# Performance work log

Measured on AMD Instinct MI355X. Metric: run time of the kernel, lower is better.

The kernel has to match this reference:

```python
import jax, jax.numpy as jnp
import numpy as np

DIM = 1024
N_HEADS = 16
HEAD_DIM = DIM // N_HEADS  # 64
B = 2
S = 2048
EPS = 1e-6  # flax LayerNorm default


def _layernorm(x, scale, bias):
    # LayerNorm over last axis with learnable scale and bias (flax defaults)
    mu = jnp.mean(x, axis=-1, keepdims=True)
    var = jnp.var(x, axis=-1, keepdims=True)
    return (x - mu) * jax.lax.rsqrt(var + EPS) * scale + bias


def _apply_rotary(t, sin, cos):
    # t: [b, s, h, hd]; sin/cos: [s, hd/2]
    tr = t.reshape(t.shape[:-1] + (-1, 2))
    r, i = tr[..., 0], tr[..., 1]            # [b, s, h, hd/2]
    c = cos[None, :, None, :]
    s_ = sin[None, :, None, :]
    out_r = r * c - i * s_
    out_i = r * s_ + i * c
    return jnp.stack([out_r, out_i], axis=-1).reshape(t.shape)


def setup_inputs() -> dict:
    key = jax.random.key(0)
    ks = jax.random.split(key, 8)
    x = jax.random.normal(ks[0], (B, S, DIM), dtype=jnp.float32)
    w_std = 1.0 / np.sqrt(DIM)  # ~lecun_normal scale
    wq = jax.random.normal(ks[1], (DIM, DIM), dtype=jnp.float32) * w_std
    wk = jax.random.normal(ks[2], (DIM, DIM), dtype=jnp.float32) * w_std
    wv = jax.random.normal(ks[3], (DIM, DIM), dtype=jnp.float32) * w_std
    wo = jax.random.normal(ks[4], (DIM, DIM), dtype=jnp.float32) * w_std
    # standard RoPE frequency table
    inv_freq = 1.0 / (10000.0 ** (np.arange(0, HEAD_DIM, 2, dtype=np.float32) / HEAD_DIM))  # [hd/2]
    angles = np.arange(S, dtype=np.float32)[:, None] * inv_freq[None, :]                    # [s, hd/2]
    return {
        "x": x,
        "freqs_sin": jnp.asarray(np.sin(angles), dtype=jnp.float32),
        "freqs_cos": jnp.asarray(np.cos(angles), dtype=jnp.float32),
        "wq": wq, "wk": wk, "wv": wv, "wo": wo,
        "q_scale": jnp.ones((DIM,), jnp.float32),
        "q_bias": jnp.zeros((DIM,), jnp.float32),
        "k_scale": jnp.ones((DIM,), jnp.float32),
        "k_bias": jnp.zeros((DIM,), jnp.float32),
    }


def reference(x, freqs_sin, freqs_cos, wq, wk, wv, wo, q_scale, q_bias, k_scale, k_bias):
    b, s, _ = x.shape
    xq = _layernorm(x @ wq, q_scale, q_bias).reshape(b, s, N_HEADS, HEAD_DIM)
    xk = _layernorm(x @ wk, k_scale, k_bias).reshape(b, s, N_HEADS, HEAD_DIM)
    xv = (x @ wv).reshape(b, s, N_HEADS, HEAD_DIM)
    xq = _apply_rotary(xq, freqs_sin, freqs_cos)
    xk = _apply_rotary(xk, freqs_sin, freqs_cos)
    scale = 1.0 / np.sqrt(HEAD_DIM)
    # non-causal SDPA, softmax in fp32 (force_fp32_for_softmax=True)
    logits = (jnp.einsum('bqhd,bkhd->bhqk', xq, xk) * scale).astype(jnp.float32)
    probs = jax.nn.softmax(logits, axis=-1).astype(xv.dtype)
    attn = jnp.einsum('bhqk,bkhd->bqhd', probs, xv).reshape(b, s, DIM)
    return attn @ wo
```

## Files before the change

kernel.cpp:

```cpp
#include <hip/hip_runtime.h>
#include <hip/hip_bf16.h>
#include <stddef.h>
#include <stdint.h>

#define DIM 1024
#define NH 16
#define HD 64
#define BATCH 2
#define SEQ 2048
#define ROWS (BATCH * SEQ)
#define KVB 128
#define NT (SEQ / KVB)

typedef short bf16x8 __attribute__((ext_vector_type(8)));
typedef float f32x4 __attribute__((ext_vector_type(4)));
typedef unsigned short u16;
typedef unsigned short u16x4v __attribute__((ext_vector_type(4)));

#define AS1 __attribute__((address_space(1)))
#define AS3 __attribute__((address_space(3)))

__device__ __forceinline__ void gload16(const u16* g, u16* l) {
  __builtin_amdgcn_global_load_lds((const AS1 void*)g, (AS3 void*)l, 16, 0, 0);
}

__device__ __forceinline__ u16 f2bf(float f) {
  union { float f; unsigned u; } v; v.f = f;
  unsigned r = v.u + 0x7FFFu + ((v.u >> 16) & 1u);
  return (u16)(r >> 16);
}

__global__ __launch_bounds__(256) void prep(
    const float* __restrict__ x, const float* __restrict__ wq,
    const float* __restrict__ wk, const float* __restrict__ wv,
    const float* __restrict__ wo, u16* __restrict__ xb,
    u16* __restrict__ wqkvT, u16* __restrict__ woT) {
  __shared__ float tile[32][33];
  int bid = blockIdx.x;
  int t = threadIdx.x;
  if (bid < 4096) {
    int i = (bid * 256 + t) * 4;
    float4 v = *(const float4*)(x + i);
    u16x4v o;
    o.x = f2bf(v.x); o.y = f2bf(v.y); o.z = f2bf(v.z); o.w = f2bf(v.w);
    *(u16x4v*)(xb + i) = o;
  } else {
    int bb = bid - 4096;
    int mat = bb >> 10;
    int tIdx = bb & 1023;
    int tr = tIdx >> 5, tc = tIdx & 31;
    const float* src = mat == 0 ? wq : mat == 1 ? wk : mat == 2 ? wv : wo;
#pragma unroll
    for (int i = 0; i < 4; ++i) {
      int idx = i * 256 + t;
      int r = idx >> 5, c = idx & 31;
      tile[r][c] = src[(tr * 32 + r) * DIM + tc * 32 + c];
    }
    __syncthreads();
    u16* dst = (mat < 3) ? (wqkvT + mat * DIM * DIM) : woT;
#pragma unroll
    for (int i = 0; i < 4; ++i) {
      int idx = i * 256 + t;
      int r = idx >> 5, c = idx & 31;
      dst[(tc * 32 + r) * DIM + tr * 32 + c] = f2bf(tile[c][r]);
    }
  }
}

__global__ __launch_bounds__(256) void gemm_bt(
    const u16* __restrict__ A, const u16* __restrict__ BT,
    float* __restrict__ C, int M, int N, int K) {
  __shared__ u16 As[128 * 32];
  __shared__ u16 Bs[128 * 32];
  int ntn = N >> 7;
  int tm = blockIdx.x / ntn, tn = blockIdx.x % ntn;
  int m0 = tm << 7, n0 = tn << 7;
  int t = threadIdx.x;
  int w = t >> 6, lane = t & 63;
  int l15 = lane & 15, l4 = lane >> 4;
  int wr = w >> 1, wc = w & 1;

  f32x4 acc[4][4];
#pragma unroll
  for (int i = 0; i < 4; ++i)
#pragma unroll
    for (int j = 0; j < 4; ++j) acc[i][j] = (f32x4){0.f, 0.f, 0.f, 0.f};

  int srow = t >> 2, scol = (t & 3) << 3;
  const u16* Ag = A + (size_t)(m0 + srow) * K + scol;
  const u16* Bg = BT + (size_t)(n0 + srow) * K + scol;
  u16* Asl = &As[t * 8];
  u16* Bsl = &Bs[t * 8];
  size_t half = (size_t)64 * K;

  for (int kt = 0; kt < K; kt += 32) {
    __syncthreads();
    gload16(Ag + kt, Asl);
    gload16(Ag + half + kt, Asl + 2048);
    gload16(Bg + kt, Bsl);
    gload16(Bg + half + kt, Bsl + 2048);
    __syncthreads();
    bf16x8 af[4], bfr[4];
#pragma unroll
    for (int i = 0; i < 4; ++i)
      af[i] = *(const bf16x8*)(&As[(wr * 64 + i * 16 + l15) * 32 + l4 * 8]);
#pragma unroll
    for (int j = 0; j < 4; ++j)
      bfr[j] = *(const bf16x8*)(&Bs[(wc * 64 + j * 16 + l15) * 32 + l4 * 8]);
#pragma unroll
    for (int i = 0; i < 4; ++i)
#pragma unroll
      for (int j = 0; j < 4; ++j)
        acc[i][j] = __builtin_amdgcn_mfma_f32_16x16x32_bf16(af[i], bfr[j],
                                                            acc[i][j], 0, 0, 0);
  }
#pragma unroll
  for (int i = 0; i < 4; ++i)
#pragma unroll
    for (int j = 0; j < 4; ++j) {
      int m = m0 + wr * 64 + i * 16 + l4 * 4;
      int n = n0 + wc * 64 + j * 16 + l15;
#pragma unroll
      for (int r = 0; r < 4; ++r) C[(size_t)(m + r) * N + n] = acc[i][j][r];
    }
}

__global__ __launch_bounds__(256) void post_qk(
    const float* __restrict__ qkv, const float* __restrict__ fsin,
    const float* __restrict__ fcos, const float* __restrict__ qsc,
    const float* __restrict__ qbi, const float* __restrict__ ksc,
    const float* __restrict__ kbi, u16* __restrict__ Q, u16* __restrict__ Kk) {
  int row = blockIdx.x;
  int b = row >> 11, s = row & 2047;
  int t = threadIdx.x;
  const float* qrow = qkv + (size_t)row * 3072;
  const float* krow = qrow + DIM;
  float4 qv = *(const float4*)(qrow + t * 4);
  float4 kv = *(const float4*)(krow + t * 4);
  float qsum = qv.x + qv.y + qv.z + qv.w;
  float qss = qv.x * qv.x + qv.y * qv.y + qv.z * qv.z + qv.w * qv.w;
  float ksum = kv.x + kv.y + kv.z + kv.w;
  float kss = kv.x * kv.x + kv.y * kv.y + kv.z * kv.z + kv.w * kv.w;
#pragma unroll
  for (int off = 1; off < 64; off <<= 1) {
    qsum += __shfl_xor(qsum, off, 64);
    qss += __shfl_xor(qss, off, 64);
    ksum += __shfl_xor(ksum, off, 64);
    kss += __shfl_xor(kss, off, 64);
  }
  __shared__ float red[4][4];
  int w = t >> 6;
  if ((t & 63) == 0) {
    red[w][0] = qsum; red[w][1] = qss; red[w][2] = ksum; red[w][3] = kss;
  }
  __syncthreads();
  qsum = red[0][0] + red[1][0] + red[2][0] + red[3][0];
  qss = red[0][1] + red[1][1] + red[2][1] + red[3][1];
  ksum = red[0][2] + red[1][2] + red[2][2] + red[3][2];
  kss = red[0][3] + red[1][3] + red[2][3] + red[3][3];
  const float inv = 1.0f / 1024.0f;
  float muq = qsum * inv;
  float rq = rsqrtf(qss * inv - muq * muq + 1e-6f);
  float muk = ksum * inv;
  float rk = rsqrtf(kss * inv - muk * muk + 1e-6f);

  int e0 = t * 4;
  int h = e0 >> 6, d0 = e0 & 63;
  float q0 = (qv.x - muq) * rq * qsc[e0 + 0] + qbi[e0 + 0];
  float q1 = (qv.y - muq) * rq * qsc[e0 + 1] + qbi[e0 + 1];
  float q2 = (qv.z - muq) * rq * qsc[e0 + 2] + qbi[e0 + 2];
  float q3 = (qv.w - muq) * rq * qsc[e0 + 3] + qbi[e0 + 3];
  float k0 = (kv.x - muk) * rk * ksc[e0 + 0] + kbi[e0 + 0];
  float k1 = (kv.y - muk) * rk * ksc[e0 + 1] + kbi[e0 + 1];
  float k2 = (kv.z - muk) * rk * ksc[e0 + 2] + kbi[e0 + 2];
  float k3 = (kv.w - muk) * rk * ksc[e0 + 3] + kbi[e0 + 3];

  int p0 = d0 >> 1;
  float c0 = fcos[s * 32 + p0], s0 = fsin[s * 32 + p0];
  float c1 = fcos[s * 32 + p0 + 1], s1 = fsin[s * 32 + p0 + 1];
  float oq0 = q0 * c0 - q1 * s0, oq1 = q0 * s0 + q1 * c0;
  float oq2 = q2 * c1 - q3 * s1, oq3 = q2 * s1 + q3 * c1;
  float ok0 = k0 * c0 - k1 * s0, ok1 = k0 * s0 + k1 * c0;
  float ok2 = k2 * c1 - k3 * s1, ok3 = k2 * s1 + k3 * c1;

  const float QSC = 0.125f * 1.44269504088896340736f;
  u16x4v qo, ko;
  qo.x = f2bf(oq0 * QSC); qo.y = f2bf(oq1 * QSC);
  qo.z = f2bf(oq2 * QSC); qo.w = f2bf(oq3 * QSC);
  ko.x = f2bf(ok0); ko.y = f2bf(ok1); ko.z = f2bf(ok2); ko.w = f2bf(ok3);
  size_t base = ((size_t)(b * NH + h) * SEQ + s) * HD + d0;
  *(u16x4v*)(Q + base) = qo;
  *(u16x4v*)(Kk + base) = ko;
}

__global__ __launch_bounds__(256) void post_v(const float* __restrict__ qkv,
                                              u16* __restrict__ Vt) {
  __shared__ u16 vt[64][65];
  int bid = blockIdx.x;
  int st = bid & 31, bh = bid >> 5;
  int b = bh >> 4, h = bh & 15;
  int t = threadIdx.x;
#pragma unroll
  for (int i = 0; i < 16; ++i) {
    int idx = i * 256 + t;
    int ss = idx >> 6, d = idx & 63;
    float v = qkv[(size_t)(b * SEQ + st * 64 + ss) * 3072 + 2048 + h * 64 + d];
    vt[ss][d] = f2bf(v);
  }
  __syncthreads();
#pragma unroll
  for (int i = 0; i < 16; ++i) {
    int idx = i * 256 + t;
    int dd = idx >> 6, ss = idx & 63;
    Vt[((size_t)bh * 64 + dd) * SEQ + st * 64 + ss] = vt[ss][dd];
  }
}

__global__ __launch_bounds__(256) void attn_fwd(const u16* __restrict__ Q,
                                                const u16* __restrict__ K,
                                                const u16* __restrict__ Vt,
                                                u16* __restrict__ O) {
  __shared__ u16 Ks[2][KVB * HD];
  __shared__ u16 Vs[2][HD * KVB];
  __shared__ u16 P[4][16][80];

  int bid0 = blockIdx.x;
  int bid = (bid0 & 7) * 128 + (bid0 >> 3);
  int qb = bid & 31, bh = bid >> 5;
  int b = bh >> 4, h = bh & 15;
  int t = threadIdx.x;
  int w = t >> 6, lane = t & 63;
  int l15 = lane & 15, l4 = lane >> 4;
  int q0 = qb * 64 + w * 16;
  const u16* Qh = Q + (size_t)bh * SEQ * HD;
  const u16* Kh = K + (size_t)bh * SEQ * HD;
  const u16* Vh = Vt + (size_t)bh * HD * SEQ;

  const u16* Kg[4];
  const u16* Vg[4];
#pragma unroll
  for (int i = 0; i < 4; ++i) {
    int c = t + 256 * i;
    int kr = c >> 3, kcol = ((c & 7) ^ (kr & 7)) << 3;
    Kg[i] = Kh + (size_t)kr * HD + kcol;
    int vr = c >> 4, vcol = ((c & 15) ^ (vr & 7)) << 3;
    Vg[i] = Vh + (size_t)vr * SEQ + vcol;
  }

#define STAGE(tile, bufi)                                  \
  do {                                                     \
    size_t j0s = (size_t)(tile) * KVB;                     \
    gload16(Kg[0] + j0s * HD, &Ks[(bufi)][(t)*8]);         \
    gload16(Kg[1] + j0s * HD, &Ks[(bufi)][(t + 256) * 8]); \
    gload16(Kg[2] + j0s * HD, &Ks[(bufi)][(t + 512) * 8]); \
    gload16(Kg[3] + j0s * HD, &Ks[(bufi)][(t + 768) * 8]); \
    gload16(Vg[0] + j0s, &Vs[(bufi)][(t)*8]);              \
    gload16(Vg[1] + j0s, &Vs[(bufi)][(t + 256) * 8]);      \
    gload16(Vg[2] + j0s, &Vs[(bufi)][(t + 512) * 8]);      \
    gload16(Vg[3] + j0s, &Vs[(bufi)][(t + 768) * 8]);      \
  } while (0)

  STAGE(0, 0);

  bf16x8 qf[2];
#pragma unroll
  for (int kf = 0; kf < 2; ++kf)
    qf[kf] = *(const bf16x8*)(Qh + (size_t)(q0 + l15) * HD + kf * 32 + l4 * 8);

  f32x4 oacc[4];
#pragma unroll
  for (int df = 0; df < 4; ++df) oacc[df] = (f32x4){0.f, 0.f, 0.f, 0.f};
  float mrun = -1e30f, lpart = 0.f;

  __syncthreads();

  int buf = 0;
  for (int it = 0; it < NT; ++it) {
    if (it + 1 < NT) STAGE(it + 1, buf ^ 1);
    const u16* Kb_ = &Ks[buf][0];
    const u16* Vb_ = &Vs[buf][0];

    f32x4 sacc[8];
#pragma unroll
    for (int nf = 0; nf < 8; ++nf) sacc[nf] = (f32x4){0.f, 0.f, 0.f, 0.f};
    __builtin_amdgcn_s_setprio(1);
#pragma unroll
    for (int nf = 0; nf < 8; ++nf) {
      int row = nf * 16 + l15;
      int swz = (row & 7) << 3;
#pragma unroll
      for (int kf = 0; kf < 2; ++kf) {
        bf16x8 kfr =
            *(const bf16x8*)(&Kb_[row * 64 + ((kf * 32 + l4 * 8) ^ swz)]);
        sacc[nf] =
            __builtin_amdgcn_mfma_f32_16x16x32_bf16(kfr, qf[kf], sacc[nf], 0, 0, 0);
      }
    }
    __builtin_amdgcn_s_setprio(0);

    bf16x8 vf[4][4];
#pragma unroll
    for (int df = 0; df < 4; ++df) {
      int row = df * 16 + l15;
      int swz = (row & 7) << 3;
#pragma unroll
      for (int kc = 0; kc < 4; ++kc)
        vf[kc][df] =
            *(const bf16x8*)(&Vb_[row * 128 + ((kc * 32 + l4 * 8) ^ swz)]);
    }

    float m16 = sacc[0][0];
#pragma unroll
    for (int nf = 0; nf < 8; ++nf)
#pragma unroll
      for (int r = 0; r < 4; ++r) m16 = fmaxf(m16, sacc[nf][r]);
    m16 = fmaxf(m16, __shfl_xor(m16, 16, 64));
    m16 = fmaxf(m16, __shfl_xor(m16, 32, 64));
    if (!__all(m16 - mrun <= 8.0f)) {
      float mnew = fmaxf(mrun, m16);
      float scl = exp2f(mrun - mnew);
      mrun = mnew;
      lpart *= scl;
      float sr[4];
#pragma unroll
      for (int r = 0; r < 4; ++r) sr[r] = __shfl(scl, l4 * 4 + r, 16);
#pragma unroll
      for (int df = 0; df < 4; ++df)
#pragma unroll
        for (int r = 0; r < 4; ++r) oacc[df][r] *= sr[r];
    }

    float rs = 0.f;
#pragma unroll
    for (int j = 0; j < 4; ++j) {
      float p0 = exp2f(sacc[j][0] - mrun);
      float p1 = exp2f(sacc[j][1] - mrun);
      float p2 = exp2f(sacc[j][2] - mrun);
      float p3 = exp2f(sacc[j][3] - mrun);
      rs += (p0 + p1) + (p2 + p3);
      __hip_bfloat162 pa, pb;
      pa.x = __float2bfloat16(p0); pa.y = __float2bfloat16(p1);
      pb.x = __float2bfloat16(p2); pb.y = __float2bfloat16(p3);
      uint2 pk2;
      pk2.x = *reinterpret_cast<unsigned int*>(&pa);
      pk2.y = *reinterpret_cast<unsigned int*>(&pb);
      *(uint2*)(&P[w][l15][j * 16 + l4 * 4]) = pk2;
    }
    asm volatile("s_waitcnt lgkmcnt(0)" ::: "memory");
    __builtin_amdgcn_sched_barrier(0);
    __builtin_amdgcn_s_setprio(1);
#pragma unroll
    for (int kc = 0; kc < 2; ++kc) {
      bf16x8 pf = *(const bf16x8*)(&P[w][l15][kc * 32 + l4 * 8]);
#pragma unroll
      for (int df = 0; df < 4; ++df)
        oacc[df] =
            __builtin_amdgcn_mfma_f32_16x16x32_bf16(pf, vf[kc][df], oacc[df], 0, 0, 0);
    }
    __builtin_amdgcn_s_setprio(0);
#pragma unroll
    for (int j = 0; j < 4; ++j) {
      float p0 = exp2f(sacc[4 + j][0] - mrun);
      float p1 = exp2f(sacc[4 + j][1] - mrun);
      float p2 = exp2f(sacc[4 + j][2] - mrun);
      float p3 = exp2f(sacc[4 + j][3] - mrun);
      rs += (p0 + p1) + (p2 + p3);
      __hip_bfloat162 pa, pb;
      pa.x = __float2bfloat16(p0); pa.y = __float2bfloat16(p1);
      pb.x = __float2bfloat16(p2); pb.y = __float2bfloat16(p3);
      uint2 pk2;
      pk2.x = *reinterpret_cast<unsigned int*>(&pa);
      pk2.y = *reinterpret_cast<unsigned int*>(&pb);
      *(uint2*)(&P[w][l15][j * 16 + l4 * 4]) = pk2;
    }
    asm volatile("s_waitcnt lgkmcnt(0)" ::: "memory");
    __builtin_amdgcn_sched_barrier(0);
    __builtin_amdgcn_s_setprio(1);
#pragma unroll
    for (int kc = 0; kc < 2; ++kc) {
      bf16x8 pf = *(const bf16x8*)(&P[w][l15][kc * 32 + l4 * 8]);
#pragma unroll
      for (int df = 0; df < 4; ++df)
        oacc[df] = __builtin_amdgcn_mfma_f32_16x16x32_bf16(pf, vf[kc + 2][df],
                                                           oacc[df], 0, 0, 0);
    }
    __builtin_amdgcn_s_setprio(0);

    lpart += rs;
    __syncthreads();
    buf ^= 1;
  }
#undef STAGE
  lpart += __shfl_xor(lpart, 16, 64);
  lpart += __shfl_xor(lpart, 32, 64);
  float lr[4];
#pragma unroll
  for (int r = 0; r < 4; ++r) lr[r] = 1.0f / __shfl(lpart, l4 * 4 + r, 16);
#pragma unroll
  for (int df = 0; df < 4; ++df) {
    int dcol = h * 64 + df * 16 + l15;
#pragma unroll
    for (int r = 0; r < 4; ++r)
      O[(size_t)(b * SEQ + q0 + l4 * 4 + r) * DIM + dcol] = f2bf(oacc[df][r] * lr[r]);
  }
}

extern "C" void kernel_launch(void* const* d_in, const int* in_sizes, int n_in,
                              void* d_out, int out_size, void* d_ws,
                              size_t ws_size, hipStream_t stream) {
  const float* x = (const float*)d_in[0];
  const float* fsin = (const float*)d_in[1];
  const float* fcos = (const float*)d_in[2];
  const float* wq = (const float*)d_in[3];
  const float* wk = (const float*)d_in[4];
  const float* wv = (const float*)d_in[5];
  const float* wo = (const float*)d_in[6];
  const float* q_scale = (const float*)d_in[7];
  const float* q_bias = (const float*)d_in[8];
  const float* k_scale = (const float*)d_in[9];
  const float* k_bias = (const float*)d_in[10];
  float* out = (float*)d_out;

  u16* xb = (u16*)d_ws;
  u16* wqkvT = xb + (size_t)ROWS * DIM;
  u16* woT = wqkvT + (size_t)3 * DIM * DIM;
  float* qkv = (float*)(woT + (size_t)DIM * DIM);
  u16* Qb = (u16*)(qkv + (size_t)ROWS * 3 * DIM);
  u16* Kb = Qb + (size_t)BATCH * NH * SEQ * HD;
  u16* Vt = Kb + (size_t)BATCH * NH * SEQ * HD;
  u16* attnb = Vt + (size_t)BATCH * NH * SEQ * HD;

  prep<<<8192, 256, 0, stream>>>(x, wq, wk, wv, wo, xb, wqkvT, woT);
  gemm_bt<<<(ROWS / 128) * (3 * DIM / 128), 256, 0, stream>>>(xb, wqkvT, qkv,
                                                              ROWS, 3 * DIM, DIM);
  post_qk<<<ROWS, 256, 0, stream>>>(qkv, fsin, fcos, q_scale, q_bias, k_scale,
                                    k_bias, Qb, Kb);
  post_v<<<BATCH * NH * (SEQ / 64), 256, 0, stream>>>(qkv, Vt);
  attn_fwd<<<BATCH * NH * (SEQ / 64), 256, 0, stream>>>(Qb, Kb, Vt, attnb);
  gemm_bt<<<(ROWS / 128) * (DIM / 128), 256, 0, stream>>>(attnb, woT, out, ROWS,
                                                          DIM, DIM);
}
```

Measured before the change: 267.1 us.

## Process two 16-row query sub-tiles per wave in attention to reuse K/V tiles

Each attention workgroup now handles 128 query rows instead of 64, with each wave computing two 16-row query subtiles. Every K fragment read from LDS now feeds two MFMAs, and V fragments are loaded in halves and shared across both subtiles. This halves the grid and the global/LDS traffic for K/V per query row. It also swaps exp2f for the raw hardware exp2 builtin. The cost is more accumulator registers (two sets of score and output tiles), which may lower occupancy, and fewer blocks to fill the GPU.

New measurement: 269.4 us. About the same (+0.9%).

```diff
diff --git a/kernel.cpp b/kernel.cpp
--- a/kernel.cpp
+++ b/kernel.cpp
@@ -225,13 +225,13 @@
   __shared__ u16 P[4][16][80];
 
   int bid0 = blockIdx.x;
-  int bid = (bid0 & 7) * 128 + (bid0 >> 3);
-  int qb = bid & 31, bh = bid >> 5;
+  int bid = (bid0 & 7) * 64 + (bid0 >> 3);
+  int qb = bid & 15, bh = bid >> 4;
   int b = bh >> 4, h = bh & 15;
   int t = threadIdx.x;
   int w = t >> 6, lane = t & 63;
   int l15 = lane & 15, l4 = lane >> 4;
-  int q0 = qb * 64 + w * 16;
+  int q0 = qb * 128 + w * 32;
   const u16* Qh = Q + (size_t)bh * SEQ * HD;
   const u16* Kh = K + (size_t)bh * SEQ * HD;
   const u16* Vh = Vt + (size_t)bh * HD * SEQ;
@@ -262,17 +262,53 @@
 
   STAGE(0, 0);
 
-  bf16x8 qf[2];
-#pragma unroll
-  for (int kf = 0; kf < 2; ++kf)
-    qf[kf] = *(const bf16x8*)(Qh + (size_t)(q0 + l15) * HD + kf * 32 + l4 * 8);
-
-  f32x4 oacc[4];
-#pragma unroll
-  for (int df = 0; df < 4; ++df) oacc[df] = (f32x4){0.f, 0.f, 0.f, 0.f};
-  float mrun = -1e30f, lpart = 0.f;
+  bf16x8 qf[2][2];
+#pragma unroll
+  for (int qs = 0; qs < 2; ++qs)
+#pragma unroll
+    for (int kf = 0; kf < 2; ++kf)
+      qf[qs][kf] = *(const bf16x8*)(Qh + (size_t)(q0 + qs * 16 + l15) * HD +
+                                    kf * 32 + l4 * 8);
+
+  f32x4 oacc[2][4];
+#pragma unroll
+  for (int qs = 0; qs < 2; ++qs)
+#pragma unroll
+    for (int df = 0; df < 4; ++df) oacc[qs][df] = (f32x4){0.f, 0.f, 0.f, 0.f};
+  float mrun[2] = {-1e30f, -1e30f};
+  float lpart[2] = {0.f, 0.f};
 
   __syncthreads();
+
+#define PHASE(qs, hb)                                                         \
+  do {                                                                        \
+    float rs = 0.f;                                                           \
+    _Pragma("unroll") for (int j = 0; j < 4; ++j) {                           \
+      float p0 = __builtin_amdgcn_exp2f(sacc[qs][(hb) + j][0] - mrun[qs]);    \
+      float p1 = __builtin_amdgcn_exp2f(sacc[qs][(hb) + j][1] - mrun[qs]);    \
+      float p2 = __builtin_amdgcn_exp2f(sacc[qs][(hb) + j][2] - mrun[qs]);    \
+      float p3 = __builtin_amdgcn_exp2f(sacc[qs][(hb) + j][3] - mrun[qs]);    \
+      rs += (p0 + p1) + (p2 + p3);                                            \
+      __hip_bfloat162 pa, pb;                                                 \
+      pa.x = __float2bfloat16(p0); pa.y = __float2bfloat16(p1);               \
+      pb.x = __float2bfloat16(p2); pb.y = __float2bfloat16(p3);               \
+      uint2 pk2;                                                              \
+      pk2.x = *reinterpret_cast<unsigned int*>(&pa);                          \
+      pk2.y = *reinterpret_cast<unsigned int*>(&pb);                          \
+      *(uint2*)(&P[w][l15][j * 16 + l4 * 4]) = pk2;                           \
+    }                                                                         \
+    lpart[qs] += rs;                                                          \
+    asm volatile("s_waitcnt lgkmcnt(0)" ::: "memory");                        \
+    __builtin_amdgcn_sched_barrier(0);                                        \
+    __builtin_amdgcn_s_setprio(1);                                            \
+    _Pragma("unroll") for (int kc = 0; kc < 2; ++kc) {                        \
+      bf16x8 pf = *(const bf16x8*)(&P[w][l15][kc * 32 + l4 * 8]);             \
+      _Pragma("unroll") for (int df = 0; df < 4; ++df)                        \
+        oacc[qs][df] = __builtin_amdgcn_mfma_f32_16x16x32_bf16(               \
+            pf, vf[kc][df], oacc[qs][df], 0, 0, 0);                           \
+    }                                                                         \
+    __builtin_amdgcn_s_setprio(0);                                            \
+  } while (0)
 
   int buf = 0;
   for (int it = 0; it < NT; ++it) {
@@ -280,9 +316,11 @@
     const u16* Kb_ = &Ks[buf][0];
     const u16* Vb_ = &Vs[buf][0];
 
-    f32x4 sacc[8];
-#pragma unroll
-    for (int nf = 0; nf < 8; ++nf) sacc[nf] = (f32x4){0.f, 0.f, 0.f, 0.f};
+    f32x4 sacc[2][8];
+#pragma unroll
+    for (int qs = 0; qs < 2; ++qs)
+#pragma unroll
+      for (int nf = 0; nf < 8; ++nf) sacc[qs][nf] = (f32x4){0.f, 0.f, 0.f, 0.f};
     __builtin_amdgcn_s_setprio(1);
 #pragma unroll
     for (int nf = 0; nf < 8; ++nf) {
@@ -292,116 +330,85 @@
       for (int kf = 0; kf < 2; ++kf) {
         bf16x8 kfr =
             *(const bf16x8*)(&Kb_[row * 64 + ((kf * 32 + l4 * 8) ^ swz)]);
-        sacc[nf] =
-            __builtin_amdgcn_mfma_f32_16x16x32_bf16(kfr, qf[kf], sacc[nf], 0, 0, 0);
+        sacc[0][nf] =
+            __builtin_amdgcn_mfma_f32_16x16x32_bf16(kfr, qf[0][kf], sacc[0][nf], 0, 0, 0);
+        sacc[1][nf] =
+            __builtin_amdgcn_mfma_f32_16x16x32_bf16(kfr, qf[1][kf], sacc[1][nf], 0, 0, 0);
       }
     }
     __builtin_amdgcn_s_setprio(0);
 
-    bf16x8 vf[4][4];
-#pragma unroll
-    for (int df = 0; df < 4; ++df) {
-      int row = df * 16 + l15;
-      int swz = (row & 7) << 3;
-#pragma unroll
-      for (int kc = 0; kc < 4; ++kc)
-        vf[kc][df] =
-            *(const bf16x8*)(&Vb_[row * 128 + ((kc * 32 + l4 * 8) ^ swz)]);
-    }
-
-    float m16 = sacc[0][0];
-#pragma unroll
-    for (int nf = 0; nf < 8; ++nf)
-#pragma unroll
-      for (int r = 0; r < 4; ++r) m16 = fmaxf(m16, sacc[nf][r]);
-    m16 = fmaxf(m16, __shfl_xor(m16, 16, 64));
-    m16 = fmaxf(m16, __shfl_xor(m16, 32, 64));
-    if (!__all(m16 - mrun <= 8.0f)) {
-      float mnew = fmaxf(mrun, m16);
-      float scl = exp2f(mrun - mnew);
-      mrun = mnew;
-      lpart *= scl;
-      float sr[4];
-#pragma unroll
-      for (int r = 0; r < 4; ++r) sr[r] = __shfl(scl, l4 * 4 + r, 16);
-#pragma unroll
-      for (int df = 0; df < 4; ++df)
-#pragma unroll
-        for (int r = 0; r < 4; ++r) oacc[df][r] *= sr[r];
-    }
-
-    float rs = 0.f;
-#pragma unroll
-    for (int j = 0; j < 4; ++j) {
-      float p0 = exp2f(sacc[j][0] - mrun);
-      float p1 = exp2f(sacc[j][1] - mrun);
-      float p2 = exp2f(sacc[j][2] - mrun);
-      float p3 = exp2f(sacc[j][3] - mrun);
-      rs += (p0 + p1) + (p2 + p3);
-      __hip_bfloat162 pa, pb;
-      pa.x = __float2bfloat16(p0); pa.y = __float2bfloat16(p1);
-      pb.x = __float2bfloat16(p2); pb.y = __float2bfloat16(p3);
-      uint2 pk2;
-      pk2.x = *reinterpret_cast<unsigned int*>(&pa);
-      pk2.y = *reinterpret_cast<unsigned int*>(&pb);
-      *(uint2*)(&P[w][l15][j * 16 + l4 * 4]) = pk2;
-    }
-    asm volatile("s_waitcnt lgkmcnt(0)" ::: "memory");
-    __builtin_amdgcn_sched_barrier(0);
-    __builtin_amdgcn_s_setprio(1);
-#pragma unroll
-    for (int kc = 0; kc < 2; ++kc) {
-      bf16x8 pf = *(const bf16x8*)(&P[w][l15][kc * 32 + l4 * 8]);
-#pragma unroll
-      for (int df = 0; df < 4; ++df)
-        oacc[df] =
-            __builtin_amdgcn_mfma_f32_16x16x32_bf16(pf, vf[kc][df], oacc[df], 0, 0, 0);
-    }
-    __builtin_amdgcn_s_setprio(0);
-#pragma unroll
-    for (int j = 0; j < 4; ++j) {
-      float p0 = exp2f(sacc[4 + j][0] - mrun);
-      float p1 = exp2f(sacc[4 + j][1] - mrun);
-      float p2 = exp2f(sacc[4 + j][2] - mrun);
-      float p3 = exp2f(sacc[4 + j][3] - mrun);
-      rs += (p0 + p1) + (p2 + p3);
-      __hip_bfloat162 pa, pb;
-      pa.x = __float2bfloat16(p0); pa.y = __float2bfloat16(p1);
-      pb.x = __float2bfloat16(p2); pb.y = __float2bfloat16(p3);
-      uint2 pk2;
-      pk2.x = *reinterpret_cast<unsigned int*>(&pa);
-      pk2.y = *reinterpret_cast<unsigned int*>(&pb);
-      *(uint2*)(&P[w][l15][j * 16 + l4 * 4]) = pk2;
-    }
-    asm volatile("s_waitcnt lgkmcnt(0)" ::: "memory");
-    __builtin_amdgcn_sched_barrier(0);
-    __builtin_amdgcn_s_setprio(1);
-#pragma unroll
-    for (int kc = 0; kc < 2; ++kc) {
-      bf16x8 pf = *(const bf16x8*)(&P[w][l15][kc * 32 + l4 * 8]);
-#pragma unroll
-      for (int df = 0; df < 4; ++df)
-        oacc[df] = __builtin_amdgcn_mfma_f32_16x16x32_bf16(pf, vf[kc + 2][df],
-                                                           oacc[df], 0, 0, 0);
-    }
-    __builtin_amdgcn_s_setprio(0);
-
-    lpart += rs;
+#pragma unroll
+    for (int qs = 0; qs < 2; ++qs) {
+      float mx = sacc[qs][0][0];
+#pragma unroll
+      for (int nf = 0; nf < 8; ++nf)
+#pragma unroll
+        for (int r = 0; r < 4; ++r) mx = fmaxf(mx, sacc[qs][nf][r]);
+      mx = fmaxf(mx, __shfl_xor(mx, 16, 64));
+      mx = fmaxf(mx, __shfl_xor(mx, 32, 64));
+      if (!__all(mx - mrun[qs] <= 8.0f)) {
+        float mnew = fmaxf(mrun[qs], mx);
+        float scl = __builtin_amdgcn_exp2f(mrun[qs] - mnew);
+        mrun[qs] = mnew;
+        lpart[qs] *= scl;
+        float sr[4];
+#pragma unroll
+        for (int r = 0; r < 4; ++r) sr[r] = __shfl(scl, l4 * 4 + r, 16);
+#pragma unroll
+        for (int df = 0; df < 4; ++df)
+#pragma unroll
+          for (int r = 0; r < 4; ++r) oacc[qs][df][r] *= sr[r];
+      }
+    }
+
+    {
+      bf16x8 vf[2][4];
+#pragma unroll
+      for (int df = 0; df < 4; ++df) {
+        int row = df * 16 + l15;
+        int swz = (row & 7) << 3;
+#pragma unroll
+        for (int kc = 0; kc < 2; ++kc)
+          vf[kc][df] =
+              *(const bf16x8*)(&Vb_[row * 128 + ((kc * 32 + l4 * 8) ^ swz)]);
+      }
+      PHASE(0, 0);
+      PHASE(1, 0);
+#pragma unroll
+      for (int df = 0; df < 4; ++df) {
+        int row = df * 16 + l15;
+        int swz = (row & 7) << 3;
+#pragma unroll
+        for (int kc = 0; kc < 2; ++kc)
+          vf[kc][df] = *(const bf16x8*)(&Vb_[row * 128 +
+                                             (((kc + 2) * 32 + l4 * 8) ^ swz)]);
+      }
+      PHASE(0, 4);
+      PHASE(1, 4);
+    }
+
     __syncthreads();
     buf ^= 1;
   }
+#undef PHASE
 #undef STAGE
-  lpart += __shfl_xor(lpart, 16, 64);
-  lpart += __shfl_xor(lpart, 32, 64);
-  float lr[4];
-#pragma unroll
-  for (int r = 0; r < 4; ++r) lr[r] = 1.0f / __shfl(lpart, l4 * 4 + r, 16);
-#pragma unroll
-  for (int df = 0; df < 4; ++df) {
-    int dcol = h * 64 + df * 16 + l15;
-#pragma unroll
-    for (int r = 0; r < 4; ++r)
-      O[(size_t)(b * SEQ + q0 + l4 * 4 + r) * DIM + dcol] = f2bf(oacc[df][r] * lr[r]);
+#pragma unroll
+  for (int qs = 0; qs < 2; ++qs) {
+    float lp = lpart[qs];
+    lp += __shfl_xor(lp, 16, 64);
+    lp += __shfl_xor(lp, 32, 64);
+    float lr[4];
+#pragma unroll
+    for (int r = 0; r < 4; ++r) lr[r] = 1.0f / __shfl(lp, l4 * 4 + r, 16);
+#pragma unroll
+    for (int df = 0; df < 4; ++df) {
+      int dcol = h * 64 + df * 16 + l15;
+#pragma unroll
+      for (int r = 0; r < 4; ++r)
+        O[(size_t)(b * SEQ + q0 + qs * 16 + l4 * 4 + r) * DIM + dcol] =
+            f2bf(oacc[qs][df][r] * lr[r]);
+    }
   }
 }
 
@@ -436,7 +443,7 @@
   post_qk<<<ROWS, 256, 0, stream>>>(qkv, fsin, fcos, q_scale, q_bias, k_scale,
                                     k_bias, Qb, Kb);
   post_v<<<BATCH * NH * (SEQ / 64), 256, 0, stream>>>(qkv, Vt);
-  attn_fwd<<<BATCH * NH * (SEQ / 64), 256, 0, stream>>>(Qb, Kb, Vt, attnb);
+  attn_fwd<<<(BATCH * NH * SEQ) / 128, 256, 0, stream>>>(Qb, Kb, Vt, attnb);
   gemm_bt<<<(ROWS / 128) * (DIM / 128), 256, 0, stream>>>(attnb, woT, out, ROWS,
                                                           DIM, DIM);
 }
```
